# Kernel optimization log

Hardware: AMD Instinct MI355X
Metric: run time of the kernel (lower is better)

The kernel has to match this reference:

```python
import jax, jax.numpy as jnp
import numpy as np

B, S, HID = 2, 2048, 2048
H, KV, D = 16, 4, 128
ROT = 64           # partial rotary dim (= cos.shape[-1])
EMB = 128          # router embedding dim
TAU, BASE = 0.4, 3.0
EPS = 1e-6


def rotate_half(x):
    h = x.shape[-1] // 2
    return jnp.concatenate([-x[..., h:], x[..., :h]], axis=-1)


def rmsnorm(x, w, eps=EPS):
    # Qwen3.5: zero-init weight, (1 + w) scaling, compute in fp32
    xf = x.astype(jnp.float32)
    o = xf * jax.lax.rsqrt(jnp.mean(xf * xf, axis=-1, keepdims=True) + eps)
    return (o * (1.0 + w.astype(jnp.float32))).astype(x.dtype)


def _rope_tables():
    inv_freq = 1.0 / (10000.0 ** (np.arange(0, ROT, 2, dtype=np.float32) / ROT))
    t = np.arange(S, dtype=np.float32)
    freqs = np.outer(t, inv_freq)                 # [S, ROT/2]
    emb = np.concatenate([freqs, freqs], axis=-1)  # [S, ROT]
    cos = np.broadcast_to(np.cos(emb), (B, S, ROT)).copy()
    sin = np.broadcast_to(np.sin(emb), (B, S, ROT)).copy()
    return jnp.asarray(cos), jnp.asarray(sin)


def setup_inputs() -> dict:
    key = jax.random.key(0)
    ks = jax.random.split(key, 10)
    sc = 0.02
    cos, sin = _rope_tables()
    return {
        "hidden_states": jax.random.normal(ks[0], (B, S, HID), jnp.float32),
        "cos": cos,
        "sin": sin,
        # projection weights stored as [in, out] (torch Linear weight transposed)
        "Wq": jax.random.normal(ks[1], (HID, H * D * 2), jnp.float32) * sc,
        "Wk": jax.random.normal(ks[2], (HID, KV * D), jnp.float32) * sc,
        "Wv": jax.random.normal(ks[3], (HID, KV * D), jnp.float32) * sc,
        "Wo": jax.random.normal(ks[4], (H * D, HID), jnp.float32) * sc,
        "q_norm_w": jnp.zeros((D,), jnp.float32),
        "k_norm_w": jnp.zeros((D,), jnp.float32),
        "Wr": jax.random.normal(ks[5], (HID, EMB), jnp.float32) * sc,   # router linear
        "Wd": jax.random.normal(ks[6], (EMB, D), jnp.float32) * sc,     # router decoder
        "ln_g": jnp.ones((EMB,), jnp.float32),
        "ln_b": jnp.zeros((EMB,), jnp.float32),
        "rnn_state": jnp.zeros((EMB,), jnp.float32),
    }


def _forward(hidden_states, cos, sin, Wq, Wk, Wv, Wo, q_norm_w, k_norm_w,
             Wr, Wd, ln_g, ln_b, rnn_state):
    b, s, _ = hidden_states.shape
    # doubled q_proj -> query + gate
    qkv = jnp.einsum('bsh,hd->bsd', hidden_states, Wq).reshape(b, s, H, 2 * D)
    q, gate = qkv[..., :D], qkv[..., D:]
    gate = gate.reshape(b, s, H * D)
    k = jnp.einsum('bsh,hd->bsd', hidden_states, Wk).reshape(b, s, KV, D)
    v = jnp.einsum('bsh,hd->bsd', hidden_states, Wv).reshape(b, s, KV, D)
    # per-head RMSNorm then [b, h, s, d]
    q = rmsnorm(q, q_norm_w).transpose(0, 2, 1, 3)
    k = rmsnorm(k, k_norm_w).transpose(0, 2, 1, 3)
    v = v.transpose(0, 2, 1, 3)

    # --- head-dim router (gumbel-sigmoid, straight-through hard round) ---
    emb = jnp.einsum('bsh,he->bse', hidden_states, Wr) + rnn_state
    mu = jnp.mean(emb, -1, keepdims=True)
    var = jnp.mean((emb - mu) ** 2, -1, keepdims=True)
    ln = (emb - mu) * jax.lax.rsqrt(var + 1e-5) * ln_g + ln_b
    logits = jnp.einsum('bse,ed->bsd', jax.nn.gelu(ln, approximate=False), Wd)
    gum = -jnp.log(jax.random.exponential(jax.random.key(42), logits.shape, jnp.float32))
    y_soft = jax.nn.sigmoid((logits + gum + BASE) / TAU)
    binary = jax.lax.stop_gradient(jnp.round(y_soft) - y_soft) + y_soft  # [b, s, D]
    mask = binary[:, None, :, :]  # broadcast over heads: [b, 1, s, D]

    q = q * mask
    k = k * mask

    # partial RoPE on first ROT dims (qk_index=None training path)
    c = cos[:, None, :, :]
    si = sin[:, None, :, :]
    def rope(x):
        xr, xp = x[..., :ROT], x[..., ROT:]
        return jnp.concatenate([xr * c + rotate_half(xr) * si, xp], axis=-1)
    q = rope(q)
    k = rope(k)

    # GQA: repeat kv heads
    rep = H // KV
    k = jnp.repeat(k, rep, axis=1)
    v = jnp.repeat(v, rep, axis=1)

    scores = jnp.einsum('bhqd,bhkd->bhqk', q, k) / np.sqrt(D).astype(np.float32)
    causal = jnp.tril(jnp.ones((s, s), bool))
    scores = jnp.where(causal, scores, jnp.finfo(jnp.float32).min)
    attn = jax.nn.softmax(scores.astype(jnp.float32), axis=-1).astype(q.dtype)
    out = jnp.einsum('bhqk,bhkd->bhqd', attn, v)
    out = out.transpose(0, 2, 1, 3).reshape(b, s, H * D)
    out = out * jax.nn.sigmoid(gate)   # output gate
    return jnp.einsum('bsd,dh->bsh', out, Wo)


def reference(hidden_states, cos, sin, Wq, Wk, Wv, Wo, q_norm_w, k_norm_w,
              Wr, Wd, ln_g, ln_b, rnn_state):
    return _forward(hidden_states, cos, sin, Wq, Wk, Wv, Wo, q_norm_w, k_norm_w,
                    Wr, Wd, ln_g, ln_b, rnn_state)
```

## Files before the change

kernel.cpp:

```cpp
#include <hip/hip_runtime.h>
#include <math.h>

typedef __bf16 bf16;
typedef bf16 bf16x8 __attribute__((ext_vector_type(8)));
typedef bf16 bf16x4 __attribute__((ext_vector_type(4)));
typedef float f32x4 __attribute__((ext_vector_type(4)));

#define BB 2
#define SS 2048
#define HIDN 2048
#define NH 16
#define NKV 4
#define DD 128
#define NROT 64
#define NPROJ 5248

__device__ __forceinline__ float waveAllReduceSum(float v) {
#pragma unroll
  for (int o = 1; o < 64; o <<= 1) v += __shfl_xor(v, o, 64);
  return v;
}

__device__ __forceinline__ int xcd_swz(int orig, int nwg) {
  return (orig & 7) * (nwg >> 3) + (orig >> 3);
}

__device__ __forceinline__ void gload16(const bf16* g, bf16* l) {
  __builtin_amdgcn_global_load_lds((const __attribute__((address_space(1))) void*)g,
                                   (__attribute__((address_space(3))) void*)l, 16, 0, 0);
}

__global__ __launch_bounds__(256) void cvt_bf16_k(const float* __restrict__ in,
                                                  bf16* __restrict__ out, int n) {
  int i = (blockIdx.x * 256 + threadIdx.x) * 8;
  if (i + 7 < n) {
    float4 v0 = *reinterpret_cast<const float4*>(in + i);
    float4 v1 = *reinterpret_cast<const float4*>(in + i + 4);
    bf16x8 o = {(bf16)v0.x, (bf16)v0.y, (bf16)v0.z, (bf16)v0.w,
                (bf16)v1.x, (bf16)v1.y, (bf16)v1.z, (bf16)v1.w};
    *reinterpret_cast<bf16x8*>(out + i) = o;
  }
}

__global__ __launch_bounds__(256) void transpose_cvt(const float* __restrict__ W,
                                                     bf16* __restrict__ WT, int K, int N,
                                                     int rowOff) {
  __shared__ bf16 tile[64][72];
  int n0 = blockIdx.x * 64, k0 = blockIdx.y * 64;
  int tx = threadIdx.x & 63, ty = threadIdx.x >> 6;
#pragma unroll
  for (int i = 0; i < 16; i++) {
    int k = ty + i * 4;
    tile[k][tx] = (bf16)W[(size_t)(k0 + k) * N + n0 + tx];
  }
  __syncthreads();
#pragma unroll
  for (int i = 0; i < 16; i++) {
    int n = ty + i * 4;
    WT[(size_t)(rowOff + n0 + n) * K + k0 + tx] = tile[tx][n];
  }
}

template <typename CT>
__global__ __launch_bounds__(256) void gemm_bt(const bf16* __restrict__ A,
                                               const bf16* __restrict__ Bt,
                                               CT* __restrict__ C, int M, int N, int K) {
  __shared__ bf16 lA[128 * 64];
  __shared__ bf16 lB[128 * 64];
  const int nbx = N >> 7;
  int wg = xcd_swz(blockIdx.x, gridDim.x);
  int bx = wg % nbx, by = wg / nbx;
  const int t = threadIdx.x;
  const int l = t & 63, w = t >> 6;
  const int wr = w >> 1, wc = w & 1;
  const int lr = l & 15, lhi = l >> 4;

  f32x4 acc[4][4];
#pragma unroll
  for (int m = 0; m < 4; m++)
#pragma unroll
    for (int n = 0; n < 4; n++) acc[m][n] = f32x4{0.f, 0.f, 0.f, 0.f};

  const int rowA0 = by * 128, rowB0 = bx * 128;
  const int nkt = K >> 6;
  for (int kt = 0; kt < nkt; ++kt) {
    __syncthreads();
#pragma unroll
    for (int it = 0; it < 4; ++it) {
      int slot = it * 256 + t;
      int row = slot >> 3, sl = slot & 7;
      gload16(A + (size_t)(rowA0 + row) * K + kt * 64 + ((sl ^ (row & 7)) << 3), lA + slot * 8);
      gload16(Bt + (size_t)(rowB0 + row) * K + kt * 64 + ((sl ^ (row & 7)) << 3), lB + slot * 8);
    }
    __syncthreads();
#pragma unroll
    for (int kc = 0; kc < 2; ++kc) {
      bf16x8 af[4], bg[4];
#pragma unroll
      for (int m = 0; m < 4; m++) {
        int row = wr * 64 + m * 16 + lr;
        af[m] = *reinterpret_cast<const bf16x8*>((char*)lA + row * 128 + (((kc * 4 + lhi) ^ (row & 7)) << 4));
      }
#pragma unroll
      for (int n = 0; n < 4; n++) {
        int row = wc * 64 + n * 16 + lr;
        bg[n] = *reinterpret_cast<const bf16x8*>((char*)lB + row * 128 + (((kc * 4 + lhi) ^ (row & 7)) << 4));
      }
      __builtin_amdgcn_s_setprio(1);
#pragma unroll
      for (int m = 0; m < 4; m++)
#pragma unroll
        for (int n = 0; n < 4; n++)
          acc[m][n] = __builtin_amdgcn_mfma_f32_16x16x32_bf16(af[m], bg[n], acc[m][n], 0, 0, 0);
      __builtin_amdgcn_s_setprio(0);
    }
  }
#pragma unroll
  for (int m = 0; m < 4; m++)
#pragma unroll
    for (int n = 0; n < 4; n++)
#pragma unroll
      for (int r = 0; r < 4; r++) {
        int grow = rowA0 + wr * 64 + m * 16 + lhi * 4 + r;
        int gcol = rowB0 + wc * 64 + n * 16 + lr;
        C[(size_t)grow * N + gcol] = (CT)acc[m][n][r];
      }
}

__device__ __forceinline__ unsigned rotl32(unsigned x, int r) { return (x << r) | (x >> (32 - r)); }

__device__ __forceinline__ float gumbel42(unsigned i) {
  const unsigned half = (unsigned)(BB * SS * DD) / 2u;
  unsigned x0, x1;
  int word;
  if (i < half) { x0 = i; x1 = i + half; word = 0; }
  else          { x0 = i - half; x1 = i; word = 1; }
  const unsigned k0 = 0u, k1 = 42u;
  const unsigned k2 = k0 ^ k1 ^ 0x1BD11BDAu;
  x0 += k0; x1 += k1;
#define TF_R(r) { x0 += x1; x1 = rotl32(x1, r); x1 ^= x0; }
  TF_R(13) TF_R(15) TF_R(26) TF_R(6)
  x0 += k1; x1 += k2 + 1u;
  TF_R(17) TF_R(29) TF_R(16) TF_R(24)
  x0 += k2; x1 += k0 + 2u;
  TF_R(13) TF_R(15) TF_R(26) TF_R(6)
  x0 += k0; x1 += k1 + 3u;
  TF_R(17) TF_R(29) TF_R(16) TF_R(24)
  x0 += k1; x1 += k2 + 4u;
  TF_R(13) TF_R(15) TF_R(26) TF_R(6)
  x0 += k2; x1 += k0 + 5u;
#undef TF_R
  unsigned bits = word ? x1 : x0;
  float u = __uint_as_float((bits >> 9) | 0x3f800000u) - 1.0f;
  float ex = -log1pf(-u);
  return -logf(ex);
}

__global__ __launch_bounds__(128) void mask_kernel(const bf16* __restrict__ qkva,
                                                   const float* __restrict__ rnn,
                                                   const float* __restrict__ lng,
                                                   const float* __restrict__ lnb,
                                                   const float* __restrict__ Wd,
                                                   bf16* __restrict__ maskb) {
  int row = blockIdx.x;
  int t = threadIdx.x;
  int l = t & 63, w = t >> 6;
  __shared__ float redm[2], redv[2], gsh[128];
  float e = (float)qkva[(size_t)row * NPROJ + 5120 + t] + rnn[t];
  float s1 = waveAllReduceSum(e);
  if (l == 0) redm[w] = s1;
  __syncthreads();
  float mu = (redm[0] + redm[1]) * (1.0f / 128.0f);
  float dv = (e - mu) * (e - mu);
  float s2 = waveAllReduceSum(dv);
  if (l == 0) redv[w] = s2;
  __syncthreads();
  float var = (redv[0] + redv[1]) * (1.0f / 128.0f);
  float ln = (e - mu) * rsqrtf(var + 1e-5f) * lng[t] + lnb[t];
  float g = 0.5f * ln * (1.0f + erff(ln * 0.7071067811865475f));
  gsh[t] = g;
  __syncthreads();
  float logit = 0.f;
#pragma unroll 8
  for (int e2 = 0; e2 < 128; e2++) logit += gsh[e2] * Wd[e2 * 128 + t];
  float gum = gumbel42((unsigned)(row * 128 + t));
  float x = (logit + gum + 3.0f) * 2.5f;
  float y = 1.0f / (1.0f + expf(-x));
  maskb[(size_t)row * 128 + t] = (bf16)rintf(y);
}

__global__ __launch_bounds__(256) void qgate_kernel(const bf16* __restrict__ qkva,
                                                    const bf16* __restrict__ maskb,
                                                    const float* __restrict__ qw,
                                                    const float* __restrict__ cosT,
                                                    const float* __restrict__ sinT,
                                                    bf16* __restrict__ wq,
                                                    bf16* __restrict__ sgate) {
  int t = threadIdx.x;
  int g = t >> 4, ln = t & 15;
  int hr = blockIdx.x * 16 + g;
  int h = hr & 15, row = hr >> 4;
  int b = row >> 11, s = row & 2047;
  const bf16* qp = qkva + (size_t)row * NPROJ + h * 256 + ln * 8;
  bf16x8 q8 = *reinterpret_cast<const bf16x8*>(qp);
  bf16x8 g8 = *reinterpret_cast<const bf16x8*>(qp + 128);
  bf16x8 m8 = *reinterpret_cast<const bf16x8*>(maskb + (size_t)row * 128 + ln * 8);
  float qf[8], ss = 0.f;
#pragma unroll
  for (int j = 0; j < 8; j++) { qf[j] = (float)q8[j]; ss += qf[j] * qf[j]; }
#pragma unroll
  for (int o = 1; o < 16; o <<= 1) ss += __shfl_xor(ss, o, 16);
  float rinv = rsqrtf(ss * (1.0f / 128.0f) + 1e-6f);
  alignas(16) float wv[8];
  const float4* qw4 = reinterpret_cast<const float4*>(qw);
  *reinterpret_cast<float4*>(&wv[0]) = qw4[ln * 2];
  *reinterpret_cast<float4*>(&wv[4]) = qw4[ln * 2 + 1];
  float qm[8];
#pragma unroll
  for (int j = 0; j < 8; j++) qm[j] = qf[j] * rinv * (1.0f + wv[j]) * (float)m8[j];
  alignas(16) float c8[8], s8[8];
  if (ln < 8) {
    const float4* c4 = reinterpret_cast<const float4*>(cosT + (size_t)row * 64);
    const float4* sn4 = reinterpret_cast<const float4*>(sinT + (size_t)row * 64);
    *reinterpret_cast<float4*>(&c8[0]) = c4[ln * 2];
    *reinterpret_cast<float4*>(&c8[4]) = c4[ln * 2 + 1];
    *reinterpret_cast<float4*>(&s8[0]) = sn4[ln * 2];
    *reinterpret_cast<float4*>(&s8[4]) = sn4[ln * 2 + 1];
  }
  float po[8];
#pragma unroll
  for (int j = 0; j < 8; j++) po[j] = __shfl_xor(qm[j], 4, 16);
  bf16x8 oq, og;
#pragma unroll
  for (int j = 0; j < 8; j++) {
    float ov;
    if (ln < 4) ov = qm[j] * c8[j] - po[j] * s8[j];
    else if (ln < 8) ov = qm[j] * c8[j] + po[j] * s8[j];
    else ov = qm[j];
    oq[j] = (bf16)(ov * 0.08838834764831845f);
    og[j] = (bf16)(1.0f / (1.0f + expf(-(float)g8[j])));
  }
  size_t o = ((size_t)((b * 16 + h) * 2048 + s)) * 128 + ln * 8;
  *reinterpret_cast<bf16x8*>(wq + o) = oq;
  *reinterpret_cast<bf16x8*>(sgate + o) = og;
}

__global__ __launch_bounds__(256) void k_kernel(const bf16* __restrict__ qkva,
                                                const bf16* __restrict__ maskb,
                                                const float* __restrict__ kw,
                                                const float* __restrict__ cosT,
                                                const float* __restrict__ sinT,
                                                bf16* __restrict__ wk) {
  int t = threadIdx.x;
  int g = t >> 4, ln = t & 15;
  int hr = blockIdx.x * 16 + g;
  int kv = hr & 3, row = hr >> 2;
  int b = row >> 11, s = row & 2047;
  const bf16* kp = qkva + (size_t)row * NPROJ + 4096 + kv * 128 + ln * 8;
  bf16x8 k8 = *reinterpret_cast<const bf16x8*>(kp);
  bf16x8 m8 = *reinterpret_cast<const bf16x8*>(maskb + (size_t)row * 128 + ln * 8);
  float kf[8], ss = 0.f;
#pragma unroll
  for (int j = 0; j < 8; j++) { kf[j] = (float)k8[j]; ss += kf[j] * kf[j]; }
#pragma unroll
  for (int o = 1; o < 16; o <<= 1) ss += __shfl_xor(ss, o, 16);
  float rinv = rsqrtf(ss * (1.0f / 128.0f) + 1e-6f);
  alignas(16) float wv[8];
  const float4* kw4 = reinterpret_cast<const float4*>(kw);
  *reinterpret_cast<float4*>(&wv[0]) = kw4[ln * 2];
  *reinterpret_cast<float4*>(&wv[4]) = kw4[ln * 2 + 1];
  float km[8];
#pragma unroll
  for (int j = 0; j < 8; j++) km[j] = kf[j] * rinv * (1.0f + wv[j]) * (float)m8[j];
  alignas(16) float c8[8], s8[8];
  if (ln < 8) {
    const float4* c4 = reinterpret_cast<const float4*>(cosT + (size_t)row * 64);
    const float4* sn4 = reinterpret_cast<const float4*>(sinT + (size_t)row * 64);
    *reinterpret_cast<float4*>(&c8[0]) = c4[ln * 2];
    *reinterpret_cast<float4*>(&c8[4]) = c4[ln * 2 + 1];
    *reinterpret_cast<float4*>(&s8[0]) = sn4[ln * 2];
    *reinterpret_cast<float4*>(&s8[4]) = sn4[ln * 2 + 1];
  }
  float po[8];
#pragma unroll
  for (int j = 0; j < 8; j++) po[j] = __shfl_xor(km[j], 4, 16);
  bf16x8 ok;
#pragma unroll
  for (int j = 0; j < 8; j++) {
    float ov;
    if (ln < 4) ov = km[j] * c8[j] - po[j] * s8[j];
    else if (ln < 8) ov = km[j] * c8[j] + po[j] * s8[j];
    else ov = km[j];
    ok[j] = (bf16)ov;
  }
  *reinterpret_cast<bf16x8*>(wk + ((size_t)((b * 4 + kv) * 2048 + s)) * 128 + ln * 8) = ok;
}

__global__ __launch_bounds__(256) void vt_kernel(const bf16* __restrict__ qkva,
                                                 bf16* __restrict__ wvt) {
  int dt = blockIdx.x & 1;
  int st = (blockIdx.x >> 1) & 31;
  int bkv = blockIdx.x >> 6;
  int b = bkv >> 2, kv = bkv & 3;
  __shared__ bf16 tl[64][72];
  int tx = threadIdx.x & 63, ty = threadIdx.x >> 6;
  int s0 = st * 64, d0 = dt * 64;
#pragma unroll
  for (int i = 0; i < 16; i++) {
    int srow = ty + i * 4;
    tl[srow][tx] = qkva[(size_t)(b * 2048 + s0 + srow) * NPROJ + 4608 + kv * 128 + d0 + tx];
  }
  __syncthreads();
#pragma unroll
  for (int i = 0; i < 16; i++) {
    int drow = ty + i * 4;
    wvt[(size_t)((b * 4 + kv) * 128 + d0 + drow) * 2048 + s0 + tx] = tl[tx][drow];
  }
}

__global__ __launch_bounds__(256) void attn_kernel(const bf16* __restrict__ wq,
                                                   const bf16* __restrict__ wk,
                                                   const bf16* __restrict__ wvt,
                                                   const bf16* __restrict__ sgate,
                                                   bf16* __restrict__ wattn) {
  __shared__ bf16 lK[2][64 * 128];
  __shared__ bf16 lV[2][128 * 64];
  __shared__ bf16 lP[4][16 * 64];
  int wg = xcd_swz(blockIdx.x, 512);
  int pair = wg & 15;
  int bh = wg >> 4;
  int b = bh >> 4, h = bh & 15, kvh = h >> 2;
  int t = threadIdx.x, l = t & 63, w = t >> 6;
  int lr = l & 15, lhi = l >> 4;

  const bf16* kbase = wk + (size_t)((b * 4 + kvh) * 2048) * 128;
  const bf16* vbase = wvt + (size_t)((b * 4 + kvh) * 128) * 2048;
  char* pb = (char*)(&lP[w][0]);

  const int qb0 = pair, qb1 = 31 - pair;
  const int n0 = qb0 + 1;

  auto stage = [&](int buf, int tt) {
#pragma unroll
    for (int it = 0; it < 4; ++it) {
      int slot = it * 256 + t;
      int row = slot >> 4, sl = slot & 15;
      gload16(kbase + (size_t)(tt * 64 + row) * 128 + ((sl ^ (row & 7)) << 3), lK[buf] + slot * 8);
      int row2 = slot >> 3, sl2 = slot & 7;
      gload16(vbase + (size_t)row2 * 2048 + tt * 64 + ((sl2 ^ (row2 & 7)) << 3), lV[buf] + slot * 8);
    }
  };

  bf16x8 aq[4];
  f32x4 oacc[8];
  float m_run, l_run;
  int half = 0, qb = qb0;

  auto load_q = [&](int qbv) {
    const bf16* qbase = wq + (size_t)((b * 16 + h) * 2048 + qbv * 64 + w * 16) * 128;
#pragma unroll
    for (int kc = 0; kc < 4; kc++)
      aq[kc] = *reinterpret_cast<const bf16x8*>(qbase + (size_t)lr * 128 + kc * 32 + lhi * 8);
  };
  load_q(qb0);
#pragma unroll
  for (int db = 0; db < 8; db++) oacc[db] = f32x4{0.f, 0.f, 0.f, 0.f};
  m_run = -3.0e38f;
  l_run = 0.f;

  stage(0, 0);
  __syncthreads();
  int cur = 0;

  for (int i = 0; i < 33; ++i) {
    int tt = (i < n0) ? i : i - n0;
    if (i + 1 < 33) {
      int tn = (i + 1 < n0) ? (i + 1) : (i + 1 - n0);
      stage(cur ^ 1, tn);
    }
    int qrow_g = qb * 64 + w * 16 + lr;

    f32x4 sacc[4];
#pragma unroll
    for (int j = 0; j < 4; j++) sacc[j] = f32x4{0.f, 0.f, 0.f, 0.f};
    __builtin_amdgcn_s_setprio(1);
#pragma unroll
    for (int kc = 0; kc < 4; kc++)
#pragma unroll
      for (int j = 0; j < 4; j++) {
        int row = j * 16 + lr;
        bf16x8 ak = *reinterpret_cast<const bf16x8*>((char*)lK[cur] + row * 256 + (((kc * 4 + lhi) ^ (row & 7)) << 4));
        sacc[j] = __builtin_amdgcn_mfma_f32_16x16x32_bf16(ak, aq[kc], sacc[j], 0, 0, 0);
      }
    __builtin_amdgcn_s_setprio(0);

    if (tt == qb) {
#pragma unroll
      for (int j = 0; j < 4; j++)
#pragma unroll
        for (int r = 0; r < 4; r++) {
          int kg = tt * 64 + j * 16 + lhi * 4 + r;
          if (kg > qrow_g) sacc[j][r] = -1e30f;
        }
    }

    float m0 = fmaxf(fmaxf(sacc[0][0], sacc[0][1]), fmaxf(sacc[0][2], sacc[0][3]));
    float m1 = fmaxf(fmaxf(sacc[1][0], sacc[1][1]), fmaxf(sacc[1][2], sacc[1][3]));
    float m2 = fmaxf(fmaxf(sacc[2][0], sacc[2][1]), fmaxf(sacc[2][2], sacc[2][3]));
    float m3 = fmaxf(fmaxf(sacc[3][0], sacc[3][1]), fmaxf(sacc[3][2], sacc[3][3]));
    float mx = fmaxf(fmaxf(m0, m1), fmaxf(m2, m3));
    mx = fmaxf(mx, __shfl_xor(mx, 16, 64));
    mx = fmaxf(mx, __shfl_xor(mx, 32, 64));

    if (!__all(mx <= m_run + 8.0f)) {
      float mnew = fmaxf(m_run, mx);
      float corr = __expf(m_run - mnew);
      l_run *= corr;
      m_run = mnew;
      float corr_o[4];
#pragma unroll
      for (int r = 0; r < 4; r++) corr_o[r] = __shfl(corr, lhi * 4 + r, 64);
#pragma unroll
      for (int db = 0; db < 8; db++)
#pragma unroll
        for (int r = 0; r < 4; r++) oacc[db][r] *= corr_o[r];
    }

    float p[4][4];
    float rs = 0.f;
#pragma unroll
    for (int j = 0; j < 4; j++) {
      float s0 = 0.f;
#pragma unroll
      for (int r = 0; r < 4; r++) {
        float pv = __expf(sacc[j][r] - m_run);
        p[j][r] = pv;
        s0 += pv;
      }
      rs += s0;
    }
    rs += __shfl_xor(rs, 16, 64);
    rs += __shfl_xor(rs, 32, 64);
    l_run += rs;

#pragma unroll
    for (int j = 0; j < 4; j++) {
      bf16x4 p4 = {(bf16)p[j][0], (bf16)p[j][1], (bf16)p[j][2], (bf16)p[j][3]};
      *reinterpret_cast<bf16x4*>(pb + lr * 128 + ((j * 32 + lhi * 8) ^ ((lr & 7) << 4))) = p4;
    }
    bf16x8 pa[2];
#pragma unroll
    for (int kc2 = 0; kc2 < 2; kc2++)
      pa[kc2] = *reinterpret_cast<const bf16x8*>(pb + lr * 128 + ((kc2 * 64 + lhi * 16) ^ ((lr & 7) << 4)));
    __builtin_amdgcn_s_setprio(1);
#pragma unroll
    for (int kc2 = 0; kc2 < 2; kc2++)
#pragma unroll
      for (int db = 0; db < 8; db++) {
        int row = db * 16 + lr;
        bf16x8 bv = *reinterpret_cast<const bf16x8*>((char*)lV[cur] + row * 128 + (((kc2 * 4 + lhi) ^ (row & 7)) << 4));
        oacc[db] = __builtin_amdgcn_mfma_f32_16x16x32_bf16(pa[kc2], bv, oacc[db], 0, 0, 0);
      }
    __builtin_amdgcn_s_setprio(0);

    if (tt == qb) {
      float linv[4];
#pragma unroll
      for (int r = 0; r < 4; r++) linv[r] = 1.0f / __shfl(l_run, lhi * 4 + r, 64);
#pragma unroll
      for (int r = 0; r < 4; r++) {
        int srow = qb * 64 + w * 16 + lhi * 4 + r;
#pragma unroll
        for (int db = 0; db < 8; db++) {
          int dcol = db * 16 + lr;
          float g = (float)sgate[(size_t)((b * 16 + h) * 2048 + srow) * 128 + dcol];
          float ov = oacc[db][r] * linv[r] * g;
          wattn[(size_t)(b * 2048 + srow) * 2048 + h * 128 + dcol] = (bf16)ov;
        }
      }
      if (half == 0) {
        half = 1;
        qb = qb1;
        load_q(qb1);
#pragma unroll
        for (int db = 0; db < 8; db++) oacc[db] = f32x4{0.f, 0.f, 0.f, 0.f};
        m_run = -3.0e38f;
        l_run = 0.f;
      }
    }

    __syncthreads();
    cur ^= 1;
  }
}

extern "C" void kernel_launch(void* const* d_in, const int* in_sizes, int n_in,
                              void* d_out, int out_size, void* d_ws, size_t ws_size,
                              hipStream_t stream) {
  const float* hidden = (const float*)d_in[0];
  const float* cosT = (const float*)d_in[1];
  const float* sinT = (const float*)d_in[2];
  const float* Wq = (const float*)d_in[3];
  const float* Wk = (const float*)d_in[4];
  const float* Wv = (const float*)d_in[5];
  const float* Wo = (const float*)d_in[6];
  const float* qw = (const float*)d_in[7];
  const float* kw = (const float*)d_in[8];
  const float* Wr = (const float*)d_in[9];
  const float* Wd = (const float*)d_in[10];
  const float* lng = (const float*)d_in[11];
  const float* lnb = (const float*)d_in[12];
  const float* rnn = (const float*)d_in[13];
  float* out = (float*)d_out;

  char* p = (char*)d_ws;
  auto alloc = [&](size_t bytes) { char* r = p; p += (bytes + 255) & ~(size_t)255; return r; };
  bf16* hb    = (bf16*)alloc((size_t)4096 * 2048 * 2);
  bf16* WTall = (bf16*)alloc((size_t)NPROJ * 2048 * 2);
  bf16* WoT   = (bf16*)alloc((size_t)2048 * 2048 * 2);
  bf16* qkva  = (bf16*)alloc((size_t)4096 * NPROJ * 2);
  bf16* maskb = (bf16*)alloc((size_t)4096 * 128 * 2);
  bf16* wqb   = (bf16*)alloc((size_t)2 * 16 * 2048 * 128 * 2);
  bf16* wkb   = (bf16*)alloc((size_t)2 * 4 * 2048 * 128 * 2);
  bf16* wvtb  = (bf16*)alloc((size_t)2 * 4 * 128 * 2048 * 2);
  bf16* sgb   = (bf16*)alloc((size_t)2 * 16 * 2048 * 128 * 2);
  bf16* wab   = (bf16*)alloc((size_t)4096 * 2048 * 2);
  if ((size_t)(p - (char*)d_ws) > ws_size) return;

  cvt_bf16_k<<<4096, 256, 0, stream>>>(hidden, hb, 4096 * 2048);
  transpose_cvt<<<dim3(64, 32), 256, 0, stream>>>(Wq, WTall, 2048, 4096, 0);
  transpose_cvt<<<dim3(8, 32), 256, 0, stream>>>(Wk, WTall, 2048, 512, 4096);
  transpose_cvt<<<dim3(8, 32), 256, 0, stream>>>(Wv, WTall, 2048, 512, 4608);
  transpose_cvt<<<dim3(2, 32), 256, 0, stream>>>(Wr, WTall, 2048, 128, 5120);
  transpose_cvt<<<dim3(32, 32), 256, 0, stream>>>(Wo, WoT, 2048, 2048, 0);

  gemm_bt<bf16><<<41 * 32, 256, 0, stream>>>(hb, WTall, qkva, 4096, NPROJ, 2048);

  mask_kernel<<<4096, 128, 0, stream>>>(qkva, rnn, lng, lnb, Wd, maskb);
  qgate_kernel<<<4096, 256, 0, stream>>>(qkva, maskb, qw, cosT, sinT, wqb, sgb);
  k_kernel<<<1024, 256, 0, stream>>>(qkva, maskb, kw, cosT, sinT, wkb);
  vt_kernel<<<512, 256, 0, stream>>>(qkva, wvtb);

  attn_kernel<<<512, 256, 0, stream>>>(wqb, wkb, wvtb, sgb, wab);

  gemm_bt<float><<<16 * 32, 256, 0, stream>>>(wab, WoT, out, 4096, 2048, 2048);
}
```

Measured before the change: 289.1 us.

## Merge prep kernels and use 128-row query blocks with exp2 softmax in attention

Combines the hidden-state conversion and all weight transposes into one launch, and the q/k/v preparation kernels into another, to cut launch count and tail gaps. The attention kernel now runs 512 threads per block over 128-row query tiles, so each staged K/V tile serves eight waves, and grid size is halved. The log2(e) factor is folded into the query scale so the softmax can use exp2f. Causal masking now applies to any tile that overlaps the diagonal. Risks include lower occupancy from the larger blocks, more masked work on diagonal tiles, and only 256 blocks in the attention grid.

Result: faster. 279.2 us (-3.4%).

```diff
diff --git a/kernel.cpp b/kernel.cpp
--- a/kernel.cpp
+++ b/kernel.cpp
@@ -30,24 +30,11 @@
                                    (__attribute__((address_space(3))) void*)l, 16, 0, 0);
 }
 
-__global__ __launch_bounds__(256) void cvt_bf16_k(const float* __restrict__ in,
-                                                  bf16* __restrict__ out, int n) {
-  int i = (blockIdx.x * 256 + threadIdx.x) * 8;
-  if (i + 7 < n) {
-    float4 v0 = *reinterpret_cast<const float4*>(in + i);
-    float4 v1 = *reinterpret_cast<const float4*>(in + i + 4);
-    bf16x8 o = {(bf16)v0.x, (bf16)v0.y, (bf16)v0.z, (bf16)v0.w,
-                (bf16)v1.x, (bf16)v1.y, (bf16)v1.z, (bf16)v1.w};
-    *reinterpret_cast<bf16x8*>(out + i) = o;
-  }
-}
-
-__global__ __launch_bounds__(256) void transpose_cvt(const float* __restrict__ W,
-                                                     bf16* __restrict__ WT, int K, int N,
-                                                     int rowOff) {
-  __shared__ bf16 tile[64][72];
-  int n0 = blockIdx.x * 64, k0 = blockIdx.y * 64;
-  int tx = threadIdx.x & 63, ty = threadIdx.x >> 6;
+__device__ __forceinline__ void do_transpose(bf16 (*tile)[72], const float* __restrict__ W,
+                                             bf16* __restrict__ WT, int K, int N, int rowOff,
+                                             int bx, int by, int t) {
+  int n0 = bx * 64, k0 = by * 64;
+  int tx = t & 63, ty = t >> 6;
 #pragma unroll
   for (int i = 0; i < 16; i++) {
     int k = ty + i * 4;
@@ -59,6 +46,38 @@
     int n = ty + i * 4;
     WT[(size_t)(rowOff + n0 + n) * K + k0 + tx] = tile[tx][n];
   }
+}
+
+__global__ __launch_bounds__(256) void prep_weights(const float* __restrict__ hidden,
+                                                    const float* __restrict__ Wq,
+                                                    const float* __restrict__ Wk,
+                                                    const float* __restrict__ Wv,
+                                                    const float* __restrict__ Wr,
+                                                    const float* __restrict__ Wo,
+                                                    bf16* __restrict__ hb,
+                                                    bf16* __restrict__ WTall,
+                                                    bf16* __restrict__ WoT) {
+  __shared__ bf16 tile[64][72];
+  int id = blockIdx.x, t = threadIdx.x;
+  if (id < 4096) {
+    int i = (id * 256 + t) * 8;
+    float4 v0 = *reinterpret_cast<const float4*>(hidden + i);
+    float4 v1 = *reinterpret_cast<const float4*>(hidden + i + 4);
+    bf16x8 o = {(bf16)v0.x, (bf16)v0.y, (bf16)v0.z, (bf16)v0.w,
+                (bf16)v1.x, (bf16)v1.y, (bf16)v1.z, (bf16)v1.w};
+    *reinterpret_cast<bf16x8*>(hb + i) = o;
+    return;
+  }
+  int id2 = id - 4096;
+  if (id2 < 2048) { do_transpose(tile, Wq, WTall, 2048, 4096, 0, id2 & 63, id2 >> 6, t); return; }
+  id2 -= 2048;
+  if (id2 < 256) { do_transpose(tile, Wk, WTall, 2048, 512, 4096, id2 & 7, id2 >> 3, t); return; }
+  id2 -= 256;
+  if (id2 < 256) { do_transpose(tile, Wv, WTall, 2048, 512, 4608, id2 & 7, id2 >> 3, t); return; }
+  id2 -= 256;
+  if (id2 < 64) { do_transpose(tile, Wr, WTall, 2048, 128, 5120, id2 & 1, id2 >> 1, t); return; }
+  id2 -= 64;
+  do_transpose(tile, Wo, WoT, 2048, 2048, 0, id2 & 31, id2 >> 5, t);
 }
 
 template <typename CT>
@@ -189,146 +208,147 @@
   maskb[(size_t)row * 128 + t] = (bf16)rintf(y);
 }
 
-__global__ __launch_bounds__(256) void qgate_kernel(const bf16* __restrict__ qkva,
-                                                    const bf16* __restrict__ maskb,
-                                                    const float* __restrict__ qw,
-                                                    const float* __restrict__ cosT,
-                                                    const float* __restrict__ sinT,
-                                                    bf16* __restrict__ wq,
-                                                    bf16* __restrict__ sgate) {
-  int t = threadIdx.x;
-  int g = t >> 4, ln = t & 15;
-  int hr = blockIdx.x * 16 + g;
-  int h = hr & 15, row = hr >> 4;
-  int b = row >> 11, s = row & 2047;
-  const bf16* qp = qkva + (size_t)row * NPROJ + h * 256 + ln * 8;
-  bf16x8 q8 = *reinterpret_cast<const bf16x8*>(qp);
-  bf16x8 g8 = *reinterpret_cast<const bf16x8*>(qp + 128);
-  bf16x8 m8 = *reinterpret_cast<const bf16x8*>(maskb + (size_t)row * 128 + ln * 8);
-  float qf[8], ss = 0.f;
-#pragma unroll
-  for (int j = 0; j < 8; j++) { qf[j] = (float)q8[j]; ss += qf[j] * qf[j]; }
-#pragma unroll
-  for (int o = 1; o < 16; o <<= 1) ss += __shfl_xor(ss, o, 16);
-  float rinv = rsqrtf(ss * (1.0f / 128.0f) + 1e-6f);
-  alignas(16) float wv[8];
-  const float4* qw4 = reinterpret_cast<const float4*>(qw);
-  *reinterpret_cast<float4*>(&wv[0]) = qw4[ln * 2];
-  *reinterpret_cast<float4*>(&wv[4]) = qw4[ln * 2 + 1];
-  float qm[8];
-#pragma unroll
-  for (int j = 0; j < 8; j++) qm[j] = qf[j] * rinv * (1.0f + wv[j]) * (float)m8[j];
-  alignas(16) float c8[8], s8[8];
-  if (ln < 8) {
-    const float4* c4 = reinterpret_cast<const float4*>(cosT + (size_t)row * 64);
-    const float4* sn4 = reinterpret_cast<const float4*>(sinT + (size_t)row * 64);
-    *reinterpret_cast<float4*>(&c8[0]) = c4[ln * 2];
-    *reinterpret_cast<float4*>(&c8[4]) = c4[ln * 2 + 1];
-    *reinterpret_cast<float4*>(&s8[0]) = sn4[ln * 2];
-    *reinterpret_cast<float4*>(&s8[4]) = sn4[ln * 2 + 1];
-  }
-  float po[8];
-#pragma unroll
-  for (int j = 0; j < 8; j++) po[j] = __shfl_xor(qm[j], 4, 16);
-  bf16x8 oq, og;
-#pragma unroll
-  for (int j = 0; j < 8; j++) {
-    float ov;
-    if (ln < 4) ov = qm[j] * c8[j] - po[j] * s8[j];
-    else if (ln < 8) ov = qm[j] * c8[j] + po[j] * s8[j];
-    else ov = qm[j];
-    oq[j] = (bf16)(ov * 0.08838834764831845f);
-    og[j] = (bf16)(1.0f / (1.0f + expf(-(float)g8[j])));
-  }
-  size_t o = ((size_t)((b * 16 + h) * 2048 + s)) * 128 + ln * 8;
-  *reinterpret_cast<bf16x8*>(wq + o) = oq;
-  *reinterpret_cast<bf16x8*>(sgate + o) = og;
-}
-
-__global__ __launch_bounds__(256) void k_kernel(const bf16* __restrict__ qkva,
+#define QSCALE (0.08838834764831845f * 1.4426950408889634f)
+
+__global__ __launch_bounds__(256) void qkv_prep(const bf16* __restrict__ qkva,
                                                 const bf16* __restrict__ maskb,
+                                                const float* __restrict__ qw,
                                                 const float* __restrict__ kw,
                                                 const float* __restrict__ cosT,
                                                 const float* __restrict__ sinT,
-                                                bf16* __restrict__ wk) {
-  int t = threadIdx.x;
-  int g = t >> 4, ln = t & 15;
-  int hr = blockIdx.x * 16 + g;
-  int kv = hr & 3, row = hr >> 2;
-  int b = row >> 11, s = row & 2047;
-  const bf16* kp = qkva + (size_t)row * NPROJ + 4096 + kv * 128 + ln * 8;
-  bf16x8 k8 = *reinterpret_cast<const bf16x8*>(kp);
-  bf16x8 m8 = *reinterpret_cast<const bf16x8*>(maskb + (size_t)row * 128 + ln * 8);
-  float kf[8], ss = 0.f;
-#pragma unroll
-  for (int j = 0; j < 8; j++) { kf[j] = (float)k8[j]; ss += kf[j] * kf[j]; }
-#pragma unroll
-  for (int o = 1; o < 16; o <<= 1) ss += __shfl_xor(ss, o, 16);
-  float rinv = rsqrtf(ss * (1.0f / 128.0f) + 1e-6f);
-  alignas(16) float wv[8];
-  const float4* kw4 = reinterpret_cast<const float4*>(kw);
-  *reinterpret_cast<float4*>(&wv[0]) = kw4[ln * 2];
-  *reinterpret_cast<float4*>(&wv[4]) = kw4[ln * 2 + 1];
-  float km[8];
-#pragma unroll
-  for (int j = 0; j < 8; j++) km[j] = kf[j] * rinv * (1.0f + wv[j]) * (float)m8[j];
-  alignas(16) float c8[8], s8[8];
-  if (ln < 8) {
-    const float4* c4 = reinterpret_cast<const float4*>(cosT + (size_t)row * 64);
-    const float4* sn4 = reinterpret_cast<const float4*>(sinT + (size_t)row * 64);
-    *reinterpret_cast<float4*>(&c8[0]) = c4[ln * 2];
-    *reinterpret_cast<float4*>(&c8[4]) = c4[ln * 2 + 1];
-    *reinterpret_cast<float4*>(&s8[0]) = sn4[ln * 2];
-    *reinterpret_cast<float4*>(&s8[4]) = sn4[ln * 2 + 1];
-  }
-  float po[8];
-#pragma unroll
-  for (int j = 0; j < 8; j++) po[j] = __shfl_xor(km[j], 4, 16);
-  bf16x8 ok;
-#pragma unroll
-  for (int j = 0; j < 8; j++) {
-    float ov;
-    if (ln < 4) ov = km[j] * c8[j] - po[j] * s8[j];
-    else if (ln < 8) ov = km[j] * c8[j] + po[j] * s8[j];
-    else ov = km[j];
-    ok[j] = (bf16)ov;
-  }
-  *reinterpret_cast<bf16x8*>(wk + ((size_t)((b * 4 + kv) * 2048 + s)) * 128 + ln * 8) = ok;
-}
-
-__global__ __launch_bounds__(256) void vt_kernel(const bf16* __restrict__ qkva,
-                                                 bf16* __restrict__ wvt) {
-  int dt = blockIdx.x & 1;
-  int st = (blockIdx.x >> 1) & 31;
-  int bkv = blockIdx.x >> 6;
-  int b = bkv >> 2, kv = bkv & 3;
-  __shared__ bf16 tl[64][72];
-  int tx = threadIdx.x & 63, ty = threadIdx.x >> 6;
-  int s0 = st * 64, d0 = dt * 64;
-#pragma unroll
-  for (int i = 0; i < 16; i++) {
-    int srow = ty + i * 4;
-    tl[srow][tx] = qkva[(size_t)(b * 2048 + s0 + srow) * NPROJ + 4608 + kv * 128 + d0 + tx];
-  }
-  __syncthreads();
-#pragma unroll
-  for (int i = 0; i < 16; i++) {
-    int drow = ty + i * 4;
-    wvt[(size_t)((b * 4 + kv) * 128 + d0 + drow) * 2048 + s0 + tx] = tl[tx][drow];
-  }
-}
-
-__global__ __launch_bounds__(256) void attn_kernel(const bf16* __restrict__ wq,
+                                                bf16* __restrict__ wq,
+                                                bf16* __restrict__ sgate,
+                                                bf16* __restrict__ wk,
+                                                bf16* __restrict__ wvt) {
+  int id = blockIdx.x, t = threadIdx.x;
+  if (id < 4096) {
+    int g = t >> 4, ln = t & 15;
+    int hr = id * 16 + g;
+    int h = hr & 15, row = hr >> 4;
+    int b = row >> 11, s = row & 2047;
+    const bf16* qp = qkva + (size_t)row * NPROJ + h * 256 + ln * 8;
+    bf16x8 q8 = *reinterpret_cast<const bf16x8*>(qp);
+    bf16x8 g8 = *reinterpret_cast<const bf16x8*>(qp + 128);
+    bf16x8 m8 = *reinterpret_cast<const bf16x8*>(maskb + (size_t)row * 128 + ln * 8);
+    float qf[8], ss = 0.f;
+#pragma unroll
+    for (int j = 0; j < 8; j++) { qf[j] = (float)q8[j]; ss += qf[j] * qf[j]; }
+#pragma unroll
+    for (int o = 1; o < 16; o <<= 1) ss += __shfl_xor(ss, o, 16);
+    float rinv = rsqrtf(ss * (1.0f / 128.0f) + 1e-6f);
+    alignas(16) float wv[8];
+    const float4* qw4 = reinterpret_cast<const float4*>(qw);
+    *reinterpret_cast<float4*>(&wv[0]) = qw4[ln * 2];
+    *reinterpret_cast<float4*>(&wv[4]) = qw4[ln * 2 + 1];
+    float qm[8];
+#pragma unroll
+    for (int j = 0; j < 8; j++) qm[j] = qf[j] * rinv * (1.0f + wv[j]) * (float)m8[j];
+    alignas(16) float c8[8], s8[8];
+    if (ln < 8) {
+      const float4* c4 = reinterpret_cast<const float4*>(cosT + (size_t)row * 64);
+      const float4* sn4 = reinterpret_cast<const float4*>(sinT + (size_t)row * 64);
+      *reinterpret_cast<float4*>(&c8[0]) = c4[ln * 2];
+      *reinterpret_cast<float4*>(&c8[4]) = c4[ln * 2 + 1];
+      *reinterpret_cast<float4*>(&s8[0]) = sn4[ln * 2];
+      *reinterpret_cast<float4*>(&s8[4]) = sn4[ln * 2 + 1];
+    }
+    float po[8];
+#pragma unroll
+    for (int j = 0; j < 8; j++) po[j] = __shfl_xor(qm[j], 4, 16);
+    bf16x8 oq, og;
+#pragma unroll
+    for (int j = 0; j < 8; j++) {
+      float ov;
+      if (ln < 4) ov = qm[j] * c8[j] - po[j] * s8[j];
+      else if (ln < 8) ov = qm[j] * c8[j] + po[j] * s8[j];
+      else ov = qm[j];
+      oq[j] = (bf16)(ov * QSCALE);
+      og[j] = (bf16)(1.0f / (1.0f + expf(-(float)g8[j])));
+    }
+    size_t o = ((size_t)((b * 16 + h) * 2048 + s)) * 128 + ln * 8;
+    *reinterpret_cast<bf16x8*>(wq + o) = oq;
+    *reinterpret_cast<bf16x8*>(sgate + o) = og;
+    return;
+  }
+  if (id < 5120) {
+    int g = t >> 4, ln = t & 15;
+    int hr = (id - 4096) * 16 + g;
+    int kv = hr & 3, row = hr >> 2;
+    int b = row >> 11, s = row & 2047;
+    const bf16* kp = qkva + (size_t)row * NPROJ + 4096 + kv * 128 + ln * 8;
+    bf16x8 k8 = *reinterpret_cast<const bf16x8*>(kp);
+    bf16x8 m8 = *reinterpret_cast<const bf16x8*>(maskb + (size_t)row * 128 + ln * 8);
+    float kf[8], ss = 0.f;
+#pragma unroll
+    for (int j = 0; j < 8; j++) { kf[j] = (float)k8[j]; ss += kf[j] * kf[j]; }
+#pragma unroll
+    for (int o = 1; o < 16; o <<= 1) ss += __shfl_xor(ss, o, 16);
+    float rinv = rsqrtf(ss * (1.0f / 128.0f) + 1e-6f);
+    alignas(16) float wv[8];
+    const float4* kw4 = reinterpret_cast<const float4*>(kw);
+    *reinterpret_cast<float4*>(&wv[0]) = kw4[ln * 2];
+    *reinterpret_cast<float4*>(&wv[4]) = kw4[ln * 2 + 1];
+    float km[8];
+#pragma unroll
+    for (int j = 0; j < 8; j++) km[j] = kf[j] * rinv * (1.0f + wv[j]) * (float)m8[j];
+    alignas(16) float c8[8], s8[8];
+    if (ln < 8) {
+      const float4* c4 = reinterpret_cast<const float4*>(cosT + (size_t)row * 64);
+      const float4* sn4 = reinterpret_cast<const float4*>(sinT + (size_t)row * 64);
+      *reinterpret_cast<float4*>(&c8[0]) = c4[ln * 2];
+      *reinterpret_cast<float4*>(&c8[4]) = c4[ln * 2 + 1];
+      *reinterpret_cast<float4*>(&s8[0]) = sn4[ln * 2];
+      *reinterpret_cast<float4*>(&s8[4]) = sn4[ln * 2 + 1];
+    }
+    float po[8];
+#pragma unroll
+    for (int j = 0; j < 8; j++) po[j] = __shfl_xor(km[j], 4, 16);
+    bf16x8 ok;
+#pragma unroll
+    for (int j = 0; j < 8; j++) {
+      float ov;
+      if (ln < 4) ov = km[j] * c8[j] - po[j] * s8[j];
+      else if (ln < 8) ov = km[j] * c8[j] + po[j] * s8[j];
+      else ov = km[j];
+      ok[j] = (bf16)ov;
+    }
+    *reinterpret_cast<bf16x8*>(wk + ((size_t)((b * 4 + kv) * 2048 + s)) * 128 + ln * 8) = ok;
+    return;
+  }
+  {
+    __shared__ bf16 tl[64][72];
+    int vb = id - 5120;
+    int dt = vb & 1;
+    int st = (vb >> 1) & 31;
+    int bkv = vb >> 6;
+    int b = bkv >> 2, kv = bkv & 3;
+    int tx = t & 63, ty = t >> 6;
+    int s0 = st * 64, d0 = dt * 64;
+#pragma unroll
+    for (int i = 0; i < 16; i++) {
+      int srow = ty + i * 4;
+      tl[srow][tx] = qkva[(size_t)(b * 2048 + s0 + srow) * NPROJ + 4608 + kv * 128 + d0 + tx];
+    }
+    __syncthreads();
+#pragma unroll
+    for (int i = 0; i < 16; i++) {
+      int drow = ty + i * 4;
+      wvt[(size_t)((b * 4 + kv) * 128 + d0 + drow) * 2048 + s0 + tx] = tl[tx][drow];
+    }
+  }
+}
+
+__global__ __launch_bounds__(512) void attn_kernel(const bf16* __restrict__ wq,
                                                    const bf16* __restrict__ wk,
                                                    const bf16* __restrict__ wvt,
                                                    const bf16* __restrict__ sgate,
                                                    bf16* __restrict__ wattn) {
   __shared__ bf16 lK[2][64 * 128];
   __shared__ bf16 lV[2][128 * 64];
-  __shared__ bf16 lP[4][16 * 64];
-  int wg = xcd_swz(blockIdx.x, 512);
-  int pair = wg & 15;
-  int bh = wg >> 4;
+  __shared__ bf16 lP[8][16 * 64];
+  int wg = xcd_swz(blockIdx.x, 256);
+  int pp = wg & 7;
+  int bh = wg >> 3;
   int b = bh >> 4, h = bh & 15, kvh = h >> 2;
   int t = threadIdx.x, l = t & 63, w = t >> 6;
   int lr = l & 15, lhi = l >> 4;
@@ -337,13 +357,12 @@
   const bf16* vbase = wvt + (size_t)((b * 4 + kvh) * 128) * 2048;
   char* pb = (char*)(&lP[w][0]);
 
-  const int qb0 = pair, qb1 = 31 - pair;
-  const int n0 = qb0 + 1;
+  const int n0 = 2 * pp + 2;
 
   auto stage = [&](int buf, int tt) {
 #pragma unroll
-    for (int it = 0; it < 4; ++it) {
-      int slot = it * 256 + t;
+    for (int it = 0; it < 2; ++it) {
+      int slot = it * 512 + t;
       int row = slot >> 4, sl = slot & 15;
       gload16(kbase + (size_t)(tt * 64 + row) * 128 + ((sl ^ (row & 7)) << 3), lK[buf] + slot * 8);
       int row2 = slot >> 3, sl2 = slot & 7;
@@ -354,15 +373,15 @@
   bf16x8 aq[4];
   f32x4 oacc[8];
   float m_run, l_run;
-  int half = 0, qb = qb0;
+  int qb128 = pp;
 
   auto load_q = [&](int qbv) {
-    const bf16* qbase = wq + (size_t)((b * 16 + h) * 2048 + qbv * 64 + w * 16) * 128;
+    const bf16* qbase = wq + (size_t)(bh * 2048 + qbv * 128 + w * 16) * 128;
 #pragma unroll
     for (int kc = 0; kc < 4; kc++)
       aq[kc] = *reinterpret_cast<const bf16x8*>(qbase + (size_t)lr * 128 + kc * 32 + lhi * 8);
   };
-  load_q(qb0);
+  load_q(pp);
 #pragma unroll
   for (int db = 0; db < 8; db++) oacc[db] = f32x4{0.f, 0.f, 0.f, 0.f};
   m_run = -3.0e38f;
@@ -372,13 +391,13 @@
   __syncthreads();
   int cur = 0;
 
-  for (int i = 0; i < 33; ++i) {
+  for (int i = 0; i < 34; ++i) {
     int tt = (i < n0) ? i : i - n0;
-    if (i + 1 < 33) {
+    if (i + 1 < 34) {
       int tn = (i + 1 < n0) ? (i + 1) : (i + 1 - n0);
       stage(cur ^ 1, tn);
     }
-    int qrow_g = qb * 64 + w * 16 + lr;
+    int qrow0 = qb128 * 128 + w * 16;
 
     f32x4 sacc[4];
 #pragma unroll
@@ -394,7 +413,8 @@
       }
     __builtin_amdgcn_s_setprio(0);
 
-    if (tt == qb) {
+    if (tt * 64 + 63 > qrow0) {
+      int qrow_g = qrow0 + lr;
 #pragma unroll
       for (int j = 0; j < 4; j++)
 #pragma unroll
@@ -414,7 +434,7 @@
 
     if (!__all(mx <= m_run + 8.0f)) {
       float mnew = fmaxf(m_run, mx);
-      float corr = __expf(m_run - mnew);
+      float corr = exp2f(m_run - mnew);
       l_run *= corr;
       m_run = mnew;
       float corr_o[4];
@@ -433,7 +453,7 @@
       float s0 = 0.f;
 #pragma unroll
       for (int r = 0; r < 4; r++) {
-        float pv = __expf(sacc[j][r] - m_run);
+        float pv = exp2f(sacc[j][r] - m_run);
         p[j][r] = pv;
         s0 += pv;
       }
@@ -463,25 +483,24 @@
       }
     __builtin_amdgcn_s_setprio(0);
 
-    if (tt == qb) {
+    if (i == n0 - 1 || i == 33) {
       float linv[4];
 #pragma unroll
       for (int r = 0; r < 4; r++) linv[r] = 1.0f / __shfl(l_run, lhi * 4 + r, 64);
 #pragma unroll
       for (int r = 0; r < 4; r++) {
-        int srow = qb * 64 + w * 16 + lhi * 4 + r;
+        int srow = qb128 * 128 + w * 16 + lhi * 4 + r;
 #pragma unroll
         for (int db = 0; db < 8; db++) {
           int dcol = db * 16 + lr;
-          float g = (float)sgate[(size_t)((b * 16 + h) * 2048 + srow) * 128 + dcol];
+          float g = (float)sgate[(size_t)(bh * 2048 + srow) * 128 + dcol];
           float ov = oacc[db][r] * linv[r] * g;
           wattn[(size_t)(b * 2048 + srow) * 2048 + h * 128 + dcol] = (bf16)ov;
         }
       }
-      if (half == 0) {
-        half = 1;
-        qb = qb1;
-        load_q(qb1);
+      if (i == n0 - 1) {
+        qb128 = 15 - pp;
+        load_q(qb128);
 #pragma unroll
         for (int db = 0; db < 8; db++) oacc[db] = f32x4{0.f, 0.f, 0.f, 0.f};
         m_run = -3.0e38f;
@@ -527,21 +546,14 @@
   bf16* wab   = (bf16*)alloc((size_t)4096 * 2048 * 2);
   if ((size_t)(p - (char*)d_ws) > ws_size) return;
 
-  cvt_bf16_k<<<4096, 256, 0, stream>>>(hidden, hb, 4096 * 2048);
-  transpose_cvt<<<dim3(64, 32), 256, 0, stream>>>(Wq, WTall, 2048, 4096, 0);
-  transpose_cvt<<<dim3(8, 32), 256, 0, stream>>>(Wk, WTall, 2048, 512, 4096);
-  transpose_cvt<<<dim3(8, 32), 256, 0, stream>>>(Wv, WTall, 2048, 512, 4608);
-  transpose_cvt<<<dim3(2, 32), 256, 0, stream>>>(Wr, WTall, 2048, 128, 5120);
-  transpose_cvt<<<dim3(32, 32), 256, 0, stream>>>(Wo, WoT, 2048, 2048, 0);
+  prep_weights<<<7744, 256, 0, stream>>>(hidden, Wq, Wk, Wv, Wr, Wo, hb, WTall, WoT);
 
   gemm_bt<bf16><<<41 * 32, 256, 0, stream>>>(hb, WTall, qkva, 4096, NPROJ, 2048);
 
   mask_kernel<<<4096, 128, 0, stream>>>(qkva, rnn, lng, lnb, Wd, maskb);
-  qgate_kernel<<<4096, 256, 0, stream>>>(qkva, maskb, qw, cosT, sinT, wqb, sgb);
-  k_kernel<<<1024, 256, 0, stream>>>(qkva, maskb, kw, cosT, sinT, wkb);
-  vt_kernel<<<512, 256, 0, stream>>>(qkva, wvtb);
-
-  attn_kernel<<<512, 256, 0, stream>>>(wqb, wkb, wvtb, sgb, wab);
+  qkv_prep<<<5632, 256, 0, stream>>>(qkva, maskb, qw, kw, cosT, sinT, wqb, sgb, wkb, wvtb);
+
+  attn_kernel<<<256, 512, 0, stream>>>(wqb, wkb, wvtb, sgb, wab);
 
   gemm_bt<float><<<16 * 32, 256, 0, stream>>>(wab, WoT, out, 4096, 2048, 2048);
 }
```
